# Optimization experiments

Measured on AMD Instinct MI355X. Metric: run time of the kernel, lower is better.

Reference implementation:

```python
import jax, jax.numpy as jnp
import numpy as np

VOCAB = 8
EMB = 128
B, L = 4, 512


def setup_inputs() -> dict:
    key = jax.random.key(0)
    k1, k2, k3, k4 = jax.random.split(key, 4)
    x = jax.random.randint(k1, (B, L), 0, VOCAB)
    table = jax.random.normal(k2, (VOCAB, EMB), dtype=jnp.float32)
    # torch Linear(2D -> D): weight [D, 2D], bias [D]; store as [2D, D] for x @ W
    W = jax.random.normal(k3, (2 * EMB, EMB), dtype=jnp.float32) * (1.0 / np.sqrt(2 * EMB))
    b = jax.random.normal(k4, (EMB,), dtype=jnp.float32) * 0.01
    return {"x": x, "table": table, "W": W, "b": b}


def reference(x, table, W, b):
    # e: [B, L, D]
    e = table[x]
    # cat([e_i, e_j]) @ W == e_i @ W1 + e_j @ W2  (algebraically identical to
    # the unsqueeze/repeat/cat/Linear in the original, without the O(L^2*2D) blowup)
    D = e.shape[-1]
    W1, W2 = W[:D], W[D:]
    pi = e @ W1          # [B, L, D] contribution from row index i
    pj = e @ W2          # [B, L, D] contribution from column index j
    out = pi[:, :, None, :] + pj[:, None, :, :] + b  # [B, L, L, D]
    return out
```

## Files before the change

### kernel.cpp

```cpp
#include <hip/hip_runtime.h>


#define VOCAB 8
#define EMB   128
#define BATCH 4
#define LEN   512

__global__ __launch_bounds__(256) void build_C(const float* __restrict__ table,
                                               const float* __restrict__ W,
                                               const float* __restrict__ bias,
                                               float* __restrict__ C) {
    __shared__ float P1[VOCAB][EMB];
    __shared__ float P2[VOCAB][EMB];
    const int t = threadIdx.x;

    for (int idx = t; idx < VOCAB * EMB; idx += 256) {
        const int v = idx >> 7;
        const int d = idx & 127;
        float s1 = 0.f, s2 = 0.f;
        #pragma unroll 8
        for (int k = 0; k < EMB; ++k) {
            const float e = table[v * EMB + k];
            s1 += e * W[k * EMB + d];
            s2 += e * W[(EMB + k) * EMB + d];
        }
        P1[v][d] = s1;
        P2[v][d] = s2 + bias[d];
    }
    __syncthreads();

    for (int idx = t; idx < VOCAB * VOCAB * EMB; idx += 256) {
        const int d  = idx & 127;
        const int vj = (idx >> 7) & 7;
        const int vi = idx >> 10;
        C[idx] = P1[vi][d] + P2[vj][d];
    }
}

__global__ __launch_bounds__(256) void write_out(const int* __restrict__ x,
                                                 const float* __restrict__ C,
                                                 float* __restrict__ out) {
    const int bi = blockIdx.x;
    const int b  = bi >> 9;
    const int i  = bi & 511;
    const int t  = threadIdx.x;
    const int dg = t & 31;
    const int js = t >> 5;

    __shared__ float4 Crow[VOCAB][EMB / 4];
    __shared__ int    xrow[LEN];

    const int* xb = x + b * LEN;
    for (int j = t; j < LEN; j += 256) xrow[j] = xb[j];

    const int vi = xb[i];

    const float4* Cv = (const float4*)(C + (size_t)vi * VOCAB * EMB);
    Crow[t >> 5][t & 31] = Cv[t];
    __syncthreads();

    float4* orow = (float4*)(out + (size_t)bi * LEN * EMB);

    #pragma unroll 4
    for (int j0 = 0; j0 < LEN; j0 += 8) {
        const int j  = j0 + js;
        const int vj = xrow[j];
        orow[(size_t)j * (EMB / 4) + dg] = Crow[vj][dg];
    }
}

extern "C" void kernel_launch(void* const* d_in, const int* in_sizes, int n_in,
                              void* d_out, int out_size, void* d_ws, size_t ws_size,
                              hipStream_t stream) {
    const int*   x     = (const int*)d_in[0];
    const float* table = (const float*)d_in[1];
    const float* W     = (const float*)d_in[2];
    const float* bias  = (const float*)d_in[3];
    float*       out   = (float*)d_out;
    float*       C     = (float*)d_ws;

    build_C<<<1, 256, 0, stream>>>(table, W, bias, C);
    write_out<<<BATCH * LEN, 256, 0, stream>>>(x, C, out);
}
```

Before: 546.7 us.

## Parallelize pair-table build across 64 blocks and use nontemporal output stores

build_C used to run as one block that computed both projections and then combined them. It now launches one block per vocab pair, and each block computes its C row directly, which spreads a small serial prologue across many CUs at the cost of redundant matvec work. write_out now writes the 512 MB output with nontemporal stores so the cache is not polluted, and its unroll factor goes from 4 to 8. The output write is bandwidth bound and dominates, so the main expected effect comes from the store path.

Result: faster. 529.4 us (-3.2%).

```diff
diff --git a/kernel.cpp b/kernel.cpp
--- a/kernel.cpp
+++ b/kernel.cpp
@@ -6,35 +6,29 @@
 #define BATCH 4
 #define LEN   512
 
-__global__ __launch_bounds__(256) void build_C(const float* __restrict__ table,
+typedef float v4f __attribute__((ext_vector_type(4)));
+
+__global__ __launch_bounds__(128) void build_C(const float* __restrict__ table,
                                                const float* __restrict__ W,
                                                const float* __restrict__ bias,
                                                float* __restrict__ C) {
-    __shared__ float P1[VOCAB][EMB];
-    __shared__ float P2[VOCAB][EMB];
-    const int t = threadIdx.x;
+    const int vi = blockIdx.x >> 3;
+    const int vj = blockIdx.x & 7;
+    const int d  = threadIdx.x;
 
-    for (int idx = t; idx < VOCAB * EMB; idx += 256) {
-        const int v = idx >> 7;
-        const int d = idx & 127;
-        float s1 = 0.f, s2 = 0.f;
-        #pragma unroll 8
-        for (int k = 0; k < EMB; ++k) {
-            const float e = table[v * EMB + k];
-            s1 += e * W[k * EMB + d];
-            s2 += e * W[(EMB + k) * EMB + d];
-        }
-        P1[v][d] = s1;
-        P2[v][d] = s2 + bias[d];
-    }
+    __shared__ float t1[EMB];
+    __shared__ float t2[EMB];
+    t1[d] = table[vi * EMB + d];
+    t2[d] = table[vj * EMB + d];
     __syncthreads();
 
-    for (int idx = t; idx < VOCAB * VOCAB * EMB; idx += 256) {
-        const int d  = idx & 127;
-        const int vj = (idx >> 7) & 7;
-        const int vi = idx >> 10;
-        C[idx] = P1[vi][d] + P2[vj][d];
+    float s = bias[d];
+    #pragma unroll 8
+    for (int k = 0; k < EMB; ++k) {
+        s += t1[k] * W[k * EMB + d];
+        s += t2[k] * W[(EMB + k) * EMB + d];
     }
+    C[(size_t)blockIdx.x * EMB + d] = s;
 }
 
 __global__ __launch_bounds__(256) void write_out(const int* __restrict__ x,
@@ -47,25 +41,26 @@
     const int dg = t & 31;
     const int js = t >> 5;
 
-    __shared__ float4 Crow[VOCAB][EMB / 4];
-    __shared__ int    xrow[LEN];
+    __shared__ v4f Crow[VOCAB][EMB / 4];
+    __shared__ int xrow[LEN];
 
     const int* xb = x + b * LEN;
     for (int j = t; j < LEN; j += 256) xrow[j] = xb[j];
 
     const int vi = xb[i];
 
-    const float4* Cv = (const float4*)(C + (size_t)vi * VOCAB * EMB);
+    const v4f* Cv = (const v4f*)(C + (size_t)vi * VOCAB * EMB);
     Crow[t >> 5][t & 31] = Cv[t];
     __syncthreads();
 
-    float4* orow = (float4*)(out + (size_t)bi * LEN * EMB);
+    v4f* orow = (v4f*)out + (size_t)bi * LEN * (EMB / 4);
 
-    #pragma unroll 4
+    #pragma unroll 8
     for (int j0 = 0; j0 < LEN; j0 += 8) {
         const int j  = j0 + js;
         const int vj = xrow[j];
-        orow[(size_t)j * (EMB / 4) + dg] = Crow[vj][dg];
+        __builtin_nontemporal_store(Crow[vj][dg],
+                                    &orow[(size_t)j * (EMB / 4) + dg]);
     }
 }
 
@@ -79,6 +74,6 @@
     float*       out   = (float*)d_out;
     float*       C     = (float*)d_ws;
 
-    build_C<<<1, 256, 0, stream>>>(table, W, bias, C);
+    build_C<<<VOCAB * VOCAB, 128, 0, stream>>>(table, W, bias, C);
     write_out<<<BATCH * LEN, 256, 0, stream>>>(x, C, out);
 }
```
